# Kernel optimization log

Measured on AMD Instinct MI355X. Metric: run time of the kernel, lower is better.

Reference implementation:

```python
import jax, jax.numpy as jnp
import numpy as np

B, F, G, L, C = 32768, 512, 16, 64, 1000  # batch, feature_dim, n_groups, labels/group, num_classes


def setup_inputs() -> dict:
    key = jax.random.key(0)
    k1, k2, k3, k4, k5 = jax.random.split(key, 5)
    features = jax.random.normal(k1, (B, F), dtype=jnp.float32)
    group_probs = jax.random.uniform(k2, (B, G), dtype=jnp.float32)
    # stacked per-group Linear heads: W[g] is the (L, F) weight of head g, b[g] its bias
    W = jax.random.normal(k3, (G, L, F), dtype=jnp.float32) / np.sqrt(F).astype(np.float32)
    b = jax.random.normal(k4, (G, L), dtype=jnp.float32) * 0.01
    # group_to_labels: label_ids[g, j] = shared class id that head g's j-th output maps to
    label_ids = jax.random.randint(k5, (G, L), 0, C, dtype=jnp.int32)
    return {"features": features, "group_probs": group_probs, "W": W, "b": b,
            "label_ids": label_ids}


def reference(features, group_probs, W, b, label_ids):
    # all per-group linear heads as one batched GEMM: [B,G,L]
    group_logits = jnp.einsum('bf,glf->bgl', features, W) + b
    # weight each group's logits by its group probability
    weighted = group_probs[:, :, None] * group_logits          # [B, G, L]
    # scatter-add into the shared logit tensor (duplicate class ids accumulate)
    flat_idx = label_ids.reshape(-1)                            # [G*L]
    logits = jnp.zeros((features.shape[0], C), dtype=features.dtype)
    logits = logits.at[:, flat_idx].add(weighted.reshape(features.shape[0], -1))
    return logits
```

## Files before the change

kernel.cpp:

```cpp
#include <hip/hip_runtime.h>
#include <stdint.h>

#define B_SZ   32768
#define F_SZ   512
#define G_SZ   16
#define L_SZ   64
#define N_COLS 1024
#define C_SZ   1000
#define M_TILE 64
#define TILES_PER_BLK 2
#define A_STRIDE 520
#define WT_STRIDE 20
#define SMEM_BYTES 81920

typedef __attribute__((ext_vector_type(8))) short short8;
typedef __attribute__((ext_vector_type(4))) float floatx4;

__device__ __forceinline__ unsigned short f2bf(float f) {
    unsigned int x = __float_as_uint(f);
    x += 0x7fffu + ((x >> 16) & 1u);
    return (unsigned short)(x >> 16);
}

__device__ __forceinline__ void barrier_lgkm() {
    __builtin_amdgcn_sched_barrier(0);
    asm volatile("s_waitcnt lgkmcnt(0)" ::: "memory");
    __builtin_amdgcn_s_barrier();
    __builtin_amdgcn_sched_barrier(0);
}

__global__ __launch_bounds__(1024) void build_csr_kernel(const int* __restrict__ label_ids,
                                                         const float* __restrict__ bias,
                                                         int* __restrict__ off,
                                                         int* __restrict__ list,
                                                         float* __restrict__ bias_p,
                                                         unsigned char* __restrict__ g_perm) {
    __shared__ int cnt[1024];
    __shared__ int cur[1024];
    const int t = threadIdx.x;
    cnt[t] = 0;
    __syncthreads();
    const int lbl = label_ids[t];
    atomicAdd(&cnt[lbl], 1);
    __syncthreads();
    int v = cnt[t];
    #pragma unroll
    for (int d = 1; d < 1024; d <<= 1) {
        int u = (t >= d) ? cnt[t - d] : 0;
        __syncthreads();
        v += u;
        cnt[t] = v;
        __syncthreads();
    }
    int ex = (t == 0) ? 0 : cnt[t - 1];
    cur[t] = ex;
    if (t <= C_SZ) off[t] = (t == 0) ? 0 : cnt[t - 1];
    __syncthreads();
    int pos = atomicAdd(&cur[lbl], 1);
    list[pos]   = t;
    bias_p[pos] = bias[t];
    g_perm[pos] = (unsigned char)(t >> 6);
}

__global__ __launch_bounds__(256) void convert_w_kernel(const float* __restrict__ W,
                                                        const int* __restrict__ list,
                                                        unsigned short* __restrict__ Wb) {
    int idx = blockIdx.x * 256 + threadIdx.x;
    int row = idx >> 7;
    int c4  = idx & 127;
    int src = list[row];
    const float4* W4 = (const float4*)W;
    float4 v = W4[src * 128 + c4];
    ushort4 u = make_ushort4(f2bf(v.x), f2bf(v.y), f2bf(v.z), f2bf(v.w));
    ((ushort4*)Wb)[idx] = u;
}

__global__ __launch_bounds__(1024, 4) void mhc_main_kernel(
        const float* __restrict__ feat,
        const float* __restrict__ gp,
        const unsigned short* __restrict__ Wb,
        const float* __restrict__ bias_p,
        const int* __restrict__ off,
        const unsigned char* __restrict__ g_perm,
        float* __restrict__ out)
{
    __shared__ __align__(16) char smem[SMEM_BYTES];
    __shared__ float gp_s[M_TILE * G_SZ];
    __shared__ float bias_s[N_COLS];
    __shared__ unsigned char g_s[N_COLS];

    unsigned short* As = (unsigned short*)smem;
    float* WT = (float*)smem;

    const int t    = threadIdx.x;
    const int wave = t >> 6;
    const int lane = t & 63;
    const int m16  = lane & 15;
    const int quad = lane >> 4;

    bias_s[t] = bias_p[t];
    g_s[t]    = g_perm[t];
    int e0 = 0, e1 = 0;
    if (t < C_SZ) { e0 = off[t]; e1 = off[t + 1]; }

    const floatx4* f4g = (const floatx4*)feat;
    floatx4 pf[8];
    float pgp = 0.f;

    #pragma unroll
    for (int it = 0; it < TILES_PER_BLK; ++it) {
        const int tile = blockIdx.x * TILES_PER_BLK + it;
        const int r0   = tile * M_TILE;

        if (it == 0) {
            gp_s[t] = gp[(size_t)r0 * G_SZ + t];
            const floatx4* f4 = f4g + (size_t)r0 * (F_SZ / 4);
            #pragma unroll
            for (int i = 0; i < 8; ++i) {
                int idx = t + i * 1024;
                int row = idx >> 7;
                int c4  = idx & 127;
                floatx4 v = f4[idx];
                ushort4 u = make_ushort4(f2bf(v[0]), f2bf(v[1]), f2bf(v[2]), f2bf(v[3]));
                *(ushort4*)(As + row * A_STRIDE + c4 * 4) = u;
            }
        } else {
            barrier_lgkm();
            gp_s[t] = pgp;
            #pragma unroll
            for (int i = 0; i < 8; ++i) {
                int idx = t + i * 1024;
                int row = idx >> 7;
                int c4  = idx & 127;
                ushort4 u = make_ushort4(f2bf(pf[i][0]), f2bf(pf[i][1]),
                                         f2bf(pf[i][2]), f2bf(pf[i][3]));
                *(ushort4*)(As + row * A_STRIDE + c4 * 4) = u;
            }
        }
        barrier_lgkm();

        const floatx4 zero = {0.f, 0.f, 0.f, 0.f};
        floatx4 acc[4][4];
        #pragma unroll
        for (int i = 0; i < 4; ++i)
            #pragma unroll
            for (int j = 0; j < 4; ++j) acc[i][j] = zero;

        const unsigned short* aBase = As + m16 * A_STRIDE + quad * 8;
        const unsigned short* bBase = Wb + (size_t)(wave * 64 + m16) * F_SZ + quad * 8;

        #pragma unroll 4
        for (int kt = 0; kt < 16; ++kt) {
            short8 a[4];
            #pragma unroll
            for (int rt = 0; rt < 4; ++rt)
                a[rt] = *(const short8*)(aBase + rt * 16 * A_STRIDE + kt * 32);
            #pragma unroll
            for (int ct = 0; ct < 4; ++ct) {
                short8 b = *(const short8*)(bBase + ct * 16 * F_SZ + kt * 32);
                #pragma unroll
                for (int rt = 0; rt < 4; ++rt)
                    acc[rt][ct] = __builtin_amdgcn_mfma_f32_16x16x32_bf16(a[rt], b, acc[rt][ct], 0, 0, 0);
            }
        }

        #pragma unroll
        for (int p = 0; p < 4; ++p) {
            if (it == 0 && p == 2) {
                size_t base = (size_t)(tile + 1) * M_TILE * (F_SZ / 4);
                #pragma unroll
                for (int i = 0; i < 4; ++i) pf[i] = f4g[base + t + i * 1024];
                pgp = gp[(size_t)(tile + 1) * M_TILE * G_SZ + t];
            }
            if (it == 0 && p == 3) {
                size_t base = (size_t)(tile + 1) * M_TILE * (F_SZ / 4);
                #pragma unroll
                for (int i = 4; i < 8; ++i) pf[i] = f4g[base + t + i * 1024];
            }
            barrier_lgkm();
            #pragma unroll
            for (int ct = 0; ct < 4; ++ct) {
                int col = wave * 64 + ct * 16 + m16;
                int g   = g_s[col];
                float bi = bias_s[col];
                floatx4 w;
                #pragma unroll
                for (int r = 0; r < 4; ++r) {
                    int rl = quad * 4 + r;
                    w[r] = gp_s[(p * 16 + rl) * G_SZ + g] * (acc[p][ct][r] + bi);
                }
                *(floatx4*)(WT + col * WT_STRIDE + quad * 4) = w;
            }
            barrier_lgkm();
            if (t < C_SZ) {
                floatx4 s0 = zero, s1 = zero, s2 = zero, s3 = zero;
                for (int j = e0; j < e1; ++j) {
                    const float* cb = WT + j * WT_STRIDE;
                    s0 += *(const floatx4*)(cb + 0);
                    s1 += *(const floatx4*)(cb + 4);
                    s2 += *(const floatx4*)(cb + 8);
                    s3 += *(const floatx4*)(cb + 12);
                }
                size_t rb = (size_t)(r0 + p * 16) * C_SZ + t;
                #pragma unroll
                for (int r = 0; r < 4; ++r) {
                    out[rb + (size_t)(r +  0) * C_SZ] = s0[r];
                    out[rb + (size_t)(r +  4) * C_SZ] = s1[r];
                    out[rb + (size_t)(r +  8) * C_SZ] = s2[r];
                    out[rb + (size_t)(r + 12) * C_SZ] = s3[r];
                }
            }
        }
    }
}

extern "C" void kernel_launch(void* const* d_in, const int* in_sizes, int n_in,
                              void* d_out, int out_size, void* d_ws, size_t ws_size,
                              hipStream_t stream) {
    const float* feat  = (const float*)d_in[0];
    const float* gp    = (const float*)d_in[1];
    const float* W     = (const float*)d_in[2];
    const float* bias  = (const float*)d_in[3];
    const int* labels  = (const int*)d_in[4];
    float* out = (float*)d_out;

    unsigned short* Wb = (unsigned short*)d_ws;
    char* base = (char*)d_ws + (1 << 20);
    int* off             = (int*)base;
    int* list            = (int*)(base + 4096);
    float* bias_p        = (float*)(base + 8192);
    unsigned char* g_prm = (unsigned char*)(base + 12288);

    build_csr_kernel<<<1, 1024, 0, stream>>>(labels, bias, off, list, bias_p, g_prm);
    convert_w_kernel<<<(N_COLS * F_SZ / 4) / 256, 256, 0, stream>>>(W, list, Wb);
    mhc_main_kernel<<<B_SZ / (M_TILE * TILES_PER_BLK), 1024, 0, stream>>>(feat, gp, Wb, bias_p, off, g_prm, out);
}
```

Baseline: 256.0 us.

## Double-buffer epilogue staging in 8-row chunks to drop a barrier per chunk

```diff
diff --git a/kernel.cpp b/kernel.cpp
--- a/kernel.cpp
+++ b/kernel.cpp
@@ -10,8 +10,9 @@
 #define M_TILE 64
 #define TILES_PER_BLK 2
 #define A_STRIDE 520
-#define WT_STRIDE 20
-#define SMEM_BYTES 81920
+#define WT8_STRIDE 12
+#define WT8_BYTES (N_COLS * WT8_STRIDE * 4)
+#define SMEM_BYTES (2 * WT8_BYTES)
 
 typedef __attribute__((ext_vector_type(8))) short short8;
 typedef __attribute__((ext_vector_type(4))) float floatx4;
@@ -97,6 +98,7 @@
     const int lane = t & 63;
     const int m16  = lane & 15;
     const int quad = lane >> 4;
+    const int r0_blk = blockIdx.x * TILES_PER_BLK * M_TILE;
 
     bias_s[t] = bias_p[t];
     g_s[t]    = g_perm[t];
@@ -106,6 +108,7 @@
     const floatx4* f4g = (const floatx4*)feat;
     floatx4 pf[8];
     float pgp = 0.f;
+    (void)r0_blk;
 
     #pragma unroll
     for (int it = 0; it < TILES_PER_BLK; ++it) {
@@ -164,50 +167,54 @@
             }
         }
 
+        barrier_lgkm();
+
         #pragma unroll
-        for (int p = 0; p < 4; ++p) {
-            if (it == 0 && p == 2) {
+        for (int p = 0; p < 8; ++p) {
+            const int rt = p >> 1;
+            const int q0 = (p & 1) * 2;
+            float* buf = WT + (p & 1) * (N_COLS * WT8_STRIDE);
+
+            if (it == 0 && p == 4) {
                 size_t base = (size_t)(tile + 1) * M_TILE * (F_SZ / 4);
                 #pragma unroll
                 for (int i = 0; i < 4; ++i) pf[i] = f4g[base + t + i * 1024];
                 pgp = gp[(size_t)(tile + 1) * M_TILE * G_SZ + t];
             }
-            if (it == 0 && p == 3) {
+            if (it == 0 && p == 6) {
                 size_t base = (size_t)(tile + 1) * M_TILE * (F_SZ / 4);
                 #pragma unroll
                 for (int i = 4; i < 8; ++i) pf[i] = f4g[base + t + i * 1024];
             }
-            barrier_lgkm();
-            #pragma unroll
-            for (int ct = 0; ct < 4; ++ct) {
-                int col = wave * 64 + ct * 16 + m16;
-                int g   = g_s[col];
-                float bi = bias_s[col];
-                floatx4 w;
-                #pragma unroll
-                for (int r = 0; r < 4; ++r) {
-                    int rl = quad * 4 + r;
-                    w[r] = gp_s[(p * 16 + rl) * G_SZ + g] * (acc[p][ct][r] + bi);
+
+            if (quad == q0 || quad == q0 + 1) {
+                const int dq = quad - q0;
+                #pragma unroll
+                for (int ct = 0; ct < 4; ++ct) {
+                    int col = wave * 64 + ct * 16 + m16;
+                    int g   = g_s[col];
+                    float bi = bias_s[col];
+                    floatx4 w;
+                    #pragma unroll
+                    for (int r = 0; r < 4; ++r)
+                        w[r] = gp_s[(p * 8 + dq * 4 + r) * G_SZ + g] * (acc[rt][ct][r] + bi);
+                    *(floatx4*)(buf + col * WT8_STRIDE + dq * 4) = w;
                 }
-                *(floatx4*)(WT + col * WT_STRIDE + quad * 4) = w;
             }
             barrier_lgkm();
             if (t < C_SZ) {
-                floatx4 s0 = zero, s1 = zero, s2 = zero, s3 = zero;
+                floatx4 s0 = zero, s1 = zero;
+                const float* cb = buf + e0 * WT8_STRIDE;
                 for (int j = e0; j < e1; ++j) {
-                    const float* cb = WT + j * WT_STRIDE;
-                    s0 += *(const floatx4*)(cb + 0);
+                    s0 += *(const floatx4*)(cb);
                     s1 += *(const floatx4*)(cb + 4);
-                    s2 += *(const floatx4*)(cb + 8);
-                    s3 += *(const floatx4*)(cb + 12);
+                    cb += WT8_STRIDE;
                 }
-                size_t rb = (size_t)(r0 + p * 16) * C_SZ + t;
+                size_t rb = (size_t)(r0 + p * 8) * C_SZ + t;
                 #pragma unroll
                 for (int r = 0; r < 4; ++r) {
-                    out[rb + (size_t)(r +  0) * C_SZ] = s0[r];
-                    out[rb + (size_t)(r +  4) * C_SZ] = s1[r];
-                    out[rb + (size_t)(r +  8) * C_SZ] = s2[r];
-                    out[rb + (size_t)(r + 12) * C_SZ] = s3[r];
+                    out[rb + (size_t)(r + 0) * C_SZ] = s0[r];
+                    out[rb + (size_t)(r + 4) * C_SZ] = s1[r];
                 }
             }
         }
```

Result: no change. 256.1 us (+0.0%).

## Scatter epilogue in 32-row chunks and use wave-shuffle scan in CSR build

Applied to the files above, without the earlier changes.

```diff
diff --git a/kernel.cpp b/kernel.cpp
--- a/kernel.cpp
+++ b/kernel.cpp
@@ -10,8 +10,8 @@
 #define M_TILE 64
 #define TILES_PER_BLK 2
 #define A_STRIDE 520
-#define WT_STRIDE 20
-#define SMEM_BYTES 81920
+#define WT32_STRIDE 36
+#define SMEM_BYTES (N_COLS * WT32_STRIDE * 4)
 
 typedef __attribute__((ext_vector_type(8))) short short8;
 typedef __attribute__((ext_vector_type(4))) float floatx4;
@@ -37,24 +37,39 @@
                                                          unsigned char* __restrict__ g_perm) {
     __shared__ int cnt[1024];
     __shared__ int cur[1024];
-    const int t = threadIdx.x;
+    __shared__ int wsum[16];
+    const int t    = threadIdx.x;
+    const int lane = t & 63;
+    const int wv   = t >> 6;
     cnt[t] = 0;
     __syncthreads();
     const int lbl = label_ids[t];
     atomicAdd(&cnt[lbl], 1);
     __syncthreads();
-    int v = cnt[t];
+    const int v = cnt[t];
+    int x = v;
     #pragma unroll
-    for (int d = 1; d < 1024; d <<= 1) {
-        int u = (t >= d) ? cnt[t - d] : 0;
-        __syncthreads();
-        v += u;
-        cnt[t] = v;
-        __syncthreads();
+    for (int d = 1; d < 64; d <<= 1) {
+        int u = __shfl_up(x, d, 64);
+        if (lane >= d) x += u;
     }
-    int ex = (t == 0) ? 0 : cnt[t - 1];
+    if (lane == 63) wsum[wv] = x;
+    __syncthreads();
+    if (t < 16) {
+        int s = wsum[t];
+        #pragma unroll
+        for (int d = 1; d < 16; d <<= 1) {
+            int u = __shfl_up(s, d, 16);
+            if (t >= d) s += u;
+        }
+        wsum[t] = s;
+    }
+    __syncthreads();
+    const int incl = x + (wv > 0 ? wsum[wv - 1] : 0);
+    const int ex   = incl - v;
     cur[t] = ex;
-    if (t <= C_SZ) off[t] = (t == 0) ? 0 : cnt[t - 1];
+    if (t < C_SZ) off[t] = ex;
+    if (t == 0)   off[C_SZ] = N_COLS;
     __syncthreads();
     int pos = atomicAdd(&cur[lbl], 1);
     list[pos]   = t;
@@ -164,52 +179,52 @@
             }
         }
 
+        barrier_lgkm();
+
         #pragma unroll
-        for (int p = 0; p < 4; ++p) {
-            if (it == 0 && p == 2) {
+        for (int p = 0; p < 2; ++p) {
+            if (it == 0 && p == 1) {
                 size_t base = (size_t)(tile + 1) * M_TILE * (F_SZ / 4);
                 #pragma unroll
-                for (int i = 0; i < 4; ++i) pf[i] = f4g[base + t + i * 1024];
+                for (int i = 0; i < 8; ++i) pf[i] = f4g[base + t + i * 1024];
                 pgp = gp[(size_t)(tile + 1) * M_TILE * G_SZ + t];
             }
-            if (it == 0 && p == 3) {
-                size_t base = (size_t)(tile + 1) * M_TILE * (F_SZ / 4);
-                #pragma unroll
-                for (int i = 4; i < 8; ++i) pf[i] = f4g[base + t + i * 1024];
-            }
-            barrier_lgkm();
             #pragma unroll
             for (int ct = 0; ct < 4; ++ct) {
                 int col = wave * 64 + ct * 16 + m16;
                 int g   = g_s[col];
                 float bi = bias_s[col];
-                floatx4 w;
-                #pragma unroll
-                for (int r = 0; r < 4; ++r) {
-                    int rl = quad * 4 + r;
-                    w[r] = gp_s[(p * 16 + rl) * G_SZ + g] * (acc[p][ct][r] + bi);
+                #pragma unroll
+                for (int h = 0; h < 2; ++h) {
+                    floatx4 w;
+                    #pragma unroll
+                    for (int r = 0; r < 4; ++r) {
+                        int rl = h * 16 + quad * 4 + r;
+                        w[r] = gp_s[(p * 32 + rl) * G_SZ + g] * (acc[p * 2 + h][ct][r] + bi);
+                    }
+                    *(floatx4*)(WT + col * WT32_STRIDE + h * 16 + quad * 4) = w;
                 }
-                *(floatx4*)(WT + col * WT_STRIDE + quad * 4) = w;
             }
             barrier_lgkm();
             if (t < C_SZ) {
-                floatx4 s0 = zero, s1 = zero, s2 = zero, s3 = zero;
+                floatx4 s[8];
+                #pragma unroll
+                for (int k = 0; k < 8; ++k) s[k] = zero;
+                const float* cb = WT + e0 * WT32_STRIDE;
                 for (int j = e0; j < e1; ++j) {
-                    const float* cb = WT + j * WT_STRIDE;
-                    s0 += *(const floatx4*)(cb + 0);
-                    s1 += *(const floatx4*)(cb + 4);
-                    s2 += *(const floatx4*)(cb + 8);
-                    s3 += *(const floatx4*)(cb + 12);
+                    #pragma unroll
+                    for (int k = 0; k < 8; ++k)
+                        s[k] += *(const floatx4*)(cb + k * 4);
+                    cb += WT32_STRIDE;
                 }
-                size_t rb = (size_t)(r0 + p * 16) * C_SZ + t;
-                #pragma unroll
-                for (int r = 0; r < 4; ++r) {
-                    out[rb + (size_t)(r +  0) * C_SZ] = s0[r];
-                    out[rb + (size_t)(r +  4) * C_SZ] = s1[r];
-                    out[rb + (size_t)(r +  8) * C_SZ] = s2[r];
-                    out[rb + (size_t)(r + 12) * C_SZ] = s3[r];
-                }
-            }
+                size_t rb = (size_t)(r0 + p * 32) * C_SZ + t;
+                #pragma unroll
+                for (int k = 0; k < 8; ++k)
+                    #pragma unroll
+                    for (int r = 0; r < 4; ++r)
+                        out[rb + (size_t)(k * 4 + r) * C_SZ] = s[k][r];
+            }
+            if (p == 0) barrier_lgkm();
         }
     }
 }
```

Result: no change. 256.7 us (+0.3%).
